# Kernel tuning notes

Hardware: AMD Instinct MI355X
Metric: run time of the kernel (lower is better)

The kernel has to match this reference:

```python
import jax, jax.numpy as jnp
import numpy as np

N = 100000      # nodes
E = 1600000     # edges
IN = 64         # in_channels
ED = 16         # edge_dim
HID = 64        # hidden_dim
L = 5           # num conv layers
MLPL = 4        # linears per GINE mlp
B = 512         # num graphs
BN_EPS = 1e-5


def _linear_init(key, fan_in, shape):
    bound = 1.0 / np.sqrt(fan_in)
    return jax.random.uniform(key, shape, jnp.float32, -bound, bound)


def setup_inputs() -> dict:
    key = jax.random.key(0)
    ks = jax.random.split(key, 12)
    x = jax.random.normal(ks[0], (N, IN), jnp.float32)
    edge_index = jax.random.randint(ks[1], (2, E), 0, N)
    batch = jnp.sort(jax.random.randint(ks[2], (N,), 0, B))
    edge_attr = jax.random.normal(ks[3], (E, ED), jnp.float32)

    node_W = _linear_init(ks[4], IN, (IN, HID))
    node_b = _linear_init(ks[5], IN, (HID,))
    edge_W = _linear_init(ks[6], ED, (ED, HID))
    edge_b = _linear_init(ks[7], ED, (HID,))
    eps_arr = jnp.zeros((L,), jnp.float32)           # train_eps init = 0
    mlp_W = _linear_init(ks[8], HID, (L, MLPL, HID, HID))
    mlp_b = _linear_init(ks[9], HID, (L, MLPL, HID))
    bn_gamma = jnp.ones((L, HID), jnp.float32)
    bn_beta = jnp.zeros((L, HID), jnp.float32)

    return dict(x=x, edge_attr=edge_attr, node_W=node_W, node_b=node_b,
                edge_W=edge_W, edge_b=edge_b, eps_arr=eps_arr,
                mlp_W=mlp_W, mlp_b=mlp_b, bn_gamma=bn_gamma, bn_beta=bn_beta,
                edge_index=edge_index, batch=batch)


def _mlp(h, Ws, bs):
    # Linear,ReLU,Linear,ReLU,Linear,ReLU,Linear (make_mlp num_layers=4)
    for i in range(MLPL):
        h = h @ Ws[i] + bs[i]
        if i < MLPL - 1:
            h = jax.nn.relu(h)
    return h


def reference(x, edge_attr, node_W, node_b, edge_W, edge_b, eps_arr,
              mlp_W, mlp_b, bn_gamma, bn_beta, edge_index, batch):
    h = x @ node_W + node_b                      # [N, HID]
    e = edge_attr @ edge_W + edge_b              # [E, HID]
    src, dst = edge_index[0], edge_index[1]      # messages src -> dst
    for l in range(L):
        h_res = h
        msg = jax.nn.relu(h[src] + e)            # [E, HID] GINE message
        aggr = jax.ops.segment_sum(msg, dst, num_segments=N)
        h = _mlp((1.0 + eps_arr[l]) * h + aggr, mlp_W[l], mlp_b[l])
        mu = h.mean(axis=0)
        var = h.var(axis=0)                      # biased, matches BN training
        h = (h - mu) * jax.lax.rsqrt(var + BN_EPS) * bn_gamma[l] + bn_beta[l]
        h = jax.nn.relu(h) + h_res
    # global mean pool
    counts = jax.ops.segment_sum(jnp.ones((h.shape[0],), h.dtype), batch, num_segments=B)
    g = jax.ops.segment_sum(h, batch, num_segments=B) / jnp.clip(counts, 1.0)[:, None]
    return g
```

## Files before the change

kernel.cpp:

```cpp
#include <hip/hip_runtime.h>

typedef unsigned short u16;
typedef unsigned int u32;
typedef __attribute__((ext_vector_type(8))) short short8_t;
typedef __attribute__((ext_vector_type(4))) float f32x4;

static_assert(sizeof(short8_t) == 16, "short8 must be 16B");

#define NN 100000
#define NE 1600000

__device__ __forceinline__ float b2f(u16 s) {
    return __builtin_bit_cast(float, ((u32)s) << 16);
}
__device__ __forceinline__ u16 f2b(float f) {
    u32 u = __builtin_bit_cast(u32, f);
    u32 r = u + 0x7fffu + ((u >> 16) & 1u);
    return (u16)(r >> 16);
}
__device__ __forceinline__ u32 pack2(float a, float b) {
    return (u32)f2b(a) | ((u32)f2b(b) << 16);
}
__device__ __forceinline__ float ldf(const void* p, size_t i, int bf) {
    return bf ? b2f(((const u16*)p)[i]) : ((const float*)p)[i];
}

__global__ void detect_kernel(const u32* __restrict__ g, int* __restrict__ flag) {
    if (threadIdx.x == 0 && blockIdx.x == 0) flag[0] = (g[0] == 0x3F803F80u) ? 1 : 0;
}

__global__ __launch_bounds__(256) void hist_kernel(const int* __restrict__ dstA,
                                                   int* __restrict__ cnt, int ne) {
    int e = blockIdx.x * 256 + threadIdx.x;
    if (e >= ne) return;
    atomicAdd(&cnt[dstA[e]], 1);
}

__global__ __launch_bounds__(256) void scanA_kernel(const int* __restrict__ cnt,
                                                    int* __restrict__ tmp,
                                                    int* __restrict__ bsum, int n) {
    __shared__ int sm[2][512];
    int t = threadIdx.x;
    int b0 = blockIdx.x * 512;
    sm[0][t] = (b0 + t < n) ? cnt[b0 + t] : 0;
    sm[0][t + 256] = (b0 + t + 256 < n) ? cnt[b0 + t + 256] : 0;
    int pp = 0;
    for (int off = 1; off < 512; off <<= 1) {
        __syncthreads();
        int j0 = t, j1 = t + 256;
        sm[pp ^ 1][j0] = sm[pp][j0] + (j0 >= off ? sm[pp][j0 - off] : 0);
        sm[pp ^ 1][j1] = sm[pp][j1] + (j1 >= off ? sm[pp][j1 - off] : 0);
        pp ^= 1;
    }
    __syncthreads();
    if (b0 + t < n) tmp[b0 + t] = sm[pp][t];
    if (b0 + t + 256 < n) tmp[b0 + t + 256] = sm[pp][t + 256];
    if (t == 0) bsum[blockIdx.x] = sm[pp][511];
}

__global__ __launch_bounds__(256) void scanB_kernel(int* __restrict__ bsum, int nb) {
    __shared__ int sm[2][256];
    int t = threadIdx.x;
    sm[0][t] = (t < nb) ? bsum[t] : 0;
    int pp = 0;
    for (int off = 1; off < 256; off <<= 1) {
        __syncthreads();
        sm[pp ^ 1][t] = sm[pp][t] + (t >= off ? sm[pp][t - off] : 0);
        pp ^= 1;
    }
    __syncthreads();
    bsum[t] = (t == 0) ? 0 : sm[pp][t - 1];
}

__global__ __launch_bounds__(256) void scanC_kernel(const int* __restrict__ tmp,
                                                    const int* __restrict__ bsum,
                                                    int* __restrict__ row_start, int n, int ne) {
    int i = blockIdx.x * 256 + threadIdx.x;
    if (i > n) return;
    if (i == n) { row_start[n] = ne; return; }
    int off = bsum[i >> 9];
    int loc = i & 511;
    row_start[i] = off + (loc ? tmp[i - 1] : 0);
}

__global__ __launch_bounds__(256) void scatter_kernel(const int* __restrict__ srcA,
                                                      const int* __restrict__ dstA,
                                                      int* __restrict__ cursor,
                                                      int* __restrict__ sperm,
                                                      int* __restrict__ eidx, int ne) {
    int e = blockIdx.x * 256 + threadIdx.x;
    if (e >= ne) return;
    int d = dstA[e];
    int pos = atomicAdd(&cursor[d], 1);
    sperm[pos] = srcA[e];
    eidx[pos] = e;
}

__global__ __launch_bounds__(256) void eperm_kernel(const void* __restrict__ edge_attr,
                                                    const void* __restrict__ eW,
                                                    const void* __restrict__ eB,
                                                    const int* __restrict__ eidx,
                                                    u16* __restrict__ ec, int ne,
                                                    const int* __restrict__ flagp) {
    int bf = flagp[0];
    int lane = threadIdx.x & 63;
    int wid = (blockIdx.x * 256 + threadIdx.x) >> 6;
    int nw = gridDim.x * 4;
    float wt[16];
#pragma unroll
    for (int k = 0; k < 16; k++) wt[k] = ldf(eW, k * 64 + lane, bf);
    float ebv = ldf(eB, lane, bf);
    for (int j = wid; j < ne; j += nw) {
        int eid = eidx[j];
        float eav = 0.f;
        if (lane < 16) eav = ldf(edge_attr, (size_t)eid * 16 + lane, bf);
        float acc = ebv;
#pragma unroll
        for (int k = 0; k < 16; k++) {
            int bits = __builtin_amdgcn_readlane(__builtin_bit_cast(int, eav), k);
            acc += __builtin_bit_cast(float, bits) * wt[k];
        }
        ec[(size_t)j * 64 + lane] = f2b(acc);
    }
}

__global__ __launch_bounds__(256) void eacopy_kernel(const void* __restrict__ edge_attr,
                                                     const int* __restrict__ eidx,
                                                     u16* __restrict__ eap, int ne,
                                                     const int* __restrict__ flagp) {
    int bf = flagp[0];
    long long t = (long long)blockIdx.x * 256 + threadIdx.x;
    if (t >= (long long)ne * 16) return;
    int j = (int)(t >> 4), c = (int)(t & 15);
    int eid = eidx[j];
    eap[(size_t)j * 16 + c] = f2b(ldf(edge_attr, (size_t)eid * 16 + c, bf));
}

template <int NLIN, bool STATS, bool INEXT, bool OUTB16>
__global__ __launch_bounds__(256) void linear64_kernel(const void* in, float* out, u16* outb,
                                                       const void* __restrict__ W, size_t w_off,
                                                       const void* __restrict__ bias,
                                                       size_t b_off, float* stats, int n,
                                                       const int* __restrict__ flagp) {
    __shared__ __align__(16) u16 Ab[2][64 * 72];
    const int bf = flagp[0];
    const int tid = threadIdx.x;
    const int base = blockIdx.x * 64;
    {
        int row = tid >> 2;
        int c0 = (tid & 3) << 4;
        int gr = base + row;
        uint4 w0 = make_uint4(0, 0, 0, 0), w1 = make_uint4(0, 0, 0, 0);
        if (gr < n) {
            if (INEXT && bf) {
                const uint4* gp = (const uint4*)((const u16*)in + (size_t)gr * 64 + c0);
                w0 = gp[0];
                w1 = gp[1];
            } else {
                const float4* gp = (const float4*)((const float*)in + (size_t)gr * 64 + c0);
                float4 q0 = gp[0], q1 = gp[1], q2 = gp[2], q3 = gp[3];
                w0.x = pack2(q0.x, q0.y); w0.y = pack2(q0.z, q0.w);
                w0.z = pack2(q1.x, q1.y); w0.w = pack2(q1.z, q1.w);
                w1.x = pack2(q2.x, q2.y); w1.y = pack2(q2.z, q2.w);
                w1.z = pack2(q3.x, q3.y); w1.w = pack2(q3.z, q3.w);
            }
        }
        uint4* lp = (uint4*)&Ab[0][row * 72 + c0];
        lp[0] = w0;
        lp[1] = w1;
    }
    __syncthreads();
    const int lane = tid & 63;
    const int w = tid >> 6;
    const int m = lane & 15;
    const int quad = lane >> 4;
    const int col = w * 16 + m;
    short8_t bfr[NLIN][2];
    float bsv[NLIN];
#pragma unroll
    for (int i = 0; i < NLIN; i++) {
        bsv[i] = ldf(bias, b_off + i * 64 + col, bf);
#pragma unroll
        for (int kk = 0; kk < 2; kk++) {
            short8_t f;
#pragma unroll
            for (int j = 0; j < 8; j++) {
                size_t idx = w_off + (size_t)i * 4096 + (size_t)(kk * 32 + quad * 8 + j) * 64 + col;
                u16 wv = bf ? ((const u16*)W)[idx] : f2b(((const float*)W)[idx]);
                f[j] = (short)wv;
            }
            bfr[i][kk] = f;
        }
    }
    int cur = 0;
#pragma unroll
    for (int i = 0; i < NLIN; i++) {
        f32x4 accT[4];
#pragma unroll
        for (int t = 0; t < 4; t++) {
            f32x4 acc;
            acc[0] = bsv[i]; acc[1] = bsv[i]; acc[2] = bsv[i]; acc[3] = bsv[i];
            int r = t * 16 + m;
            const u16* ap = &Ab[cur][r * 72 + quad * 8];
            short8_t a0 = *(const short8_t*)ap;
            short8_t a1 = *(const short8_t*)(ap + 32);
            acc = __builtin_amdgcn_mfma_f32_16x16x32_bf16(a0, bfr[i][0], acc, 0, 0, 0);
            acc = __builtin_amdgcn_mfma_f32_16x16x32_bf16(a1, bfr[i][1], acc, 0, 0, 0);
            accT[t] = acc;
        }
        if (i < NLIN - 1) {
#pragma unroll
            for (int t = 0; t < 4; t++)
#pragma unroll
                for (int reg = 0; reg < 4; reg++) {
                    int r2 = t * 16 + quad * 4 + reg;
                    Ab[cur ^ 1][r2 * 72 + col] = f2b(fmaxf(accT[t][reg], 0.f));
                }
            __syncthreads();
            cur ^= 1;
        } else {
            float s1 = 0.f, s2 = 0.f;
#pragma unroll
            for (int t = 0; t < 4; t++)
#pragma unroll
                for (int reg = 0; reg < 4; reg++) {
                    int gr = base + t * 16 + quad * 4 + reg;
                    if (gr < n) {
                        float v = accT[t][reg];
                        out[(size_t)gr * 64 + col] = v;
                        if (OUTB16) outb[(size_t)gr * 64 + col] = f2b(v);
                        if (STATS) { s1 += v; s2 += v * v; }
                    }
                }
            if (STATS) {
                s1 += __shfl_xor(s1, 16, 64);
                s2 += __shfl_xor(s2, 16, 64);
                s1 += __shfl_xor(s1, 32, 64);
                s2 += __shfl_xor(s2, 32, 64);
                if (quad == 0) {
                    atomicAdd(&stats[col], s1);
                    atomicAdd(&stats[64 + col], s2);
                }
            }
        }
    }
}

template <bool EC>
__global__ __launch_bounds__(256) void agg_kernel(const float* __restrict__ h,
                                                  const u16* __restrict__ hb,
                                                  const u16* __restrict__ ec,
                                                  const int* __restrict__ sperm,
                                                  const int* __restrict__ row_start,
                                                  const void* __restrict__ eps_arr, int layer,
                                                  float* __restrict__ u, int n,
                                                  const void* __restrict__ eW,
                                                  const void* __restrict__ eB,
                                                  const int* __restrict__ flagp) {
    int bf = flagp[0];
    int lane = threadIdx.x & 63;
    int i = blockIdx.x * 4 + (threadIdx.x >> 6);
    if (i >= n) return;
    float wt[16];
    float ebv = 0.f;
    if (!EC) {
#pragma unroll
        for (int k = 0; k < 16; k++) wt[k] = ldf(eW, k * 64 + lane, bf);
        ebv = ldf(eB, lane, bf);
    }
    int beg = row_start[i], end = row_start[i + 1];
    float acc = 0.f;
    if (EC) {
        int p = beg;
        for (; p + 1 < end; p += 2) {
            int s0 = sperm[p], s1 = sperm[p + 1];
            float h0 = b2f(hb[(size_t)s0 * 64 + lane]);
            float h1 = b2f(hb[(size_t)s1 * 64 + lane]);
            float e0 = b2f(ec[(size_t)p * 64 + lane]);
            float e1 = b2f(ec[(size_t)p * 64 + 64 + lane]);
            acc += fmaxf(h0 + e0, 0.f);
            acc += fmaxf(h1 + e1, 0.f);
        }
        if (p < end) {
            int s0 = sperm[p];
            acc += fmaxf(b2f(hb[(size_t)s0 * 64 + lane]) + b2f(ec[(size_t)p * 64 + lane]), 0.f);
        }
    } else {
        for (int p = beg; p < end; ++p) {
            int s0 = sperm[p];
            float hv = b2f(hb[(size_t)s0 * 64 + lane]);
            float eav = 0.f;
            if (lane < 16) eav = b2f(ec[(size_t)p * 16 + lane]);
            float ev = ebv;
#pragma unroll
            for (int k = 0; k < 16; k++) {
                int bits = __builtin_amdgcn_readlane(__builtin_bit_cast(int, eav), k);
                ev += __builtin_bit_cast(float, bits) * wt[k];
            }
            acc += fmaxf(hv + ev, 0.f);
        }
    }
    float eps = 1.f + ldf(eps_arr, layer, bf);
    u[(size_t)i * 64 + lane] = eps * h[(size_t)i * 64 + lane] + acc;
}

__global__ __launch_bounds__(256) void bnres_kernel(const float* __restrict__ v,
                                                    float* __restrict__ h, u16* __restrict__ hb,
                                                    const float* __restrict__ stats,
                                                    const void* __restrict__ gamma,
                                                    const void* __restrict__ beta, size_t g_off,
                                                    int n, const int* __restrict__ flagp) {
    int bf = flagp[0];
    int idx = blockIdx.x * 256 + threadIdx.x;
    if (idx >= n * 64) return;
    int f = idx & 63;
    float inv = 1.f / (float)n;
    float mu = stats[f] * inv;
    float var = stats[64 + f] * inv - mu * mu;
    float rs = rsqrtf(var + 1e-5f);
    float ga = ldf(gamma, g_off + f, bf), be = ldf(beta, g_off + f, bf);
    float y = (v[idx] - mu) * rs * ga + be;
    float hn = fmaxf(y, 0.f) + h[idx];
    h[idx] = hn;
    hb[idx] = f2b(hn);
}

__global__ __launch_bounds__(256) void pool1_kernel(const float* __restrict__ h,
                                                    const int* __restrict__ batch,
                                                    float* __restrict__ gsum,
                                                    float* __restrict__ gcnt, int n) {
    int lane = threadIdx.x & 63;
    int s = blockIdx.x * 4 + (threadIdx.x >> 6);
    int start = s * 256;
    if (start >= n) return;
    int endn = min(start + 256, n);
    int cur = -1;
    float acc = 0.f, c = 0.f;
    for (int m = start; m < endn; ++m) {
        int b = batch[m];
        if (b != cur) {
            if (cur >= 0) {
                atomicAdd(&gsum[cur * 64 + lane], acc);
                if (lane == 0) atomicAdd(&gcnt[cur], c);
            }
            cur = b;
            acc = 0.f;
            c = 0.f;
        }
        acc += h[(size_t)m * 64 + lane];
        c += 1.f;
    }
    if (cur >= 0) {
        atomicAdd(&gsum[cur * 64 + lane], acc);
        if (lane == 0) atomicAdd(&gcnt[cur], c);
    }
}

__global__ __launch_bounds__(256) void pool2_kernel(const float* __restrict__ gsum,
                                                    const float* __restrict__ gcnt,
                                                    float* __restrict__ out) {
    int idx = blockIdx.x * 256 + threadIdx.x;
    if (idx >= 512 * 64) return;
    int b = idx >> 6;
    out[idx] = gsum[idx] / fmaxf(gcnt[b], 1.f);
}

extern "C" void kernel_launch(void* const* d_in, const int* in_sizes, int n_in, void* d_out,
                              int out_size, void* d_ws, size_t ws_size, hipStream_t stream) {
    const int N = NN, E = NE;
    const void* x = d_in[0];
    const void* edge_attr = d_in[1];
    const void* node_W = d_in[2];
    const void* node_b = d_in[3];
    const void* edge_W = d_in[4];
    const void* edge_b = d_in[5];
    const void* eps_arr = d_in[6];
    const void* mlp_W = d_in[7];
    const void* mlp_b = d_in[8];
    const void* bn_gamma = d_in[9];
    const void* bn_beta = d_in[10];
    const int* edge_index = (const int*)d_in[11];
    const int* batch = (const int*)d_in[12];

    char* ws = (char*)d_ws;
    size_t o = 0;
    auto take = [&](size_t bytes) -> size_t {
        size_t r = o;
        o = (o + bytes + 255) & ~(size_t)255;
        return r;
    };
    size_t cnt_o = take((size_t)N * 4);
    size_t stats_o = take(5 * 128 * 4);
    size_t gsum_o = take(512 * 64 * 4);
    size_t gcnt_o = take(512 * 4);
    size_t zero_len = o;
    size_t flag_o = take(256);
    size_t row_o = take((size_t)(N + 1) * 4);
    size_t tmp_o = take((size_t)N * 4);
    size_t bsum_o = take(256 * 4);
    size_t cur_o = take((size_t)N * 4);
    size_t sperm_o = take((size_t)E * 4);
    size_t eidx_o = take((size_t)E * 4);
    size_t h_o = take((size_t)N * 64 * 4);
    size_t hb_o = take((size_t)N * 64 * 2);
    size_t u_o = take((size_t)N * 64 * 4);
    size_t ec_o = o;
    bool EC = ws_size >= ec_o + (size_t)E * 64 * 2;

    int* cnt = (int*)(ws + cnt_o);
    float* stats = (float*)(ws + stats_o);
    float* gsum = (float*)(ws + gsum_o);
    float* gcnt = (float*)(ws + gcnt_o);
    int* flagp = (int*)(ws + flag_o);
    int* row = (int*)(ws + row_o);
    int* tmp = (int*)(ws + tmp_o);
    int* bsum = (int*)(ws + bsum_o);
    int* curs = (int*)(ws + cur_o);
    int* sperm = (int*)(ws + sperm_o);
    int* eidx = (int*)(ws + eidx_o);
    float* h = (float*)(ws + h_o);
    u16* hb = (u16*)(ws + hb_o);
    float* u = (float*)(ws + u_o);
    u16* ecache = (u16*)(ws + ec_o);

    hipMemsetAsync(ws, 0, zero_len, stream);
    detect_kernel<<<1, 64, 0, stream>>>((const u32*)bn_gamma, flagp);
    const int* srcA = edge_index;
    const int* dstA = edge_index + E;

    hist_kernel<<<E / 256, 256, 0, stream>>>(dstA, cnt, E);
    int nb = (N + 511) / 512;
    scanA_kernel<<<nb, 256, 0, stream>>>(cnt, tmp, bsum, N);
    scanB_kernel<<<1, 256, 0, stream>>>(bsum, nb);
    scanC_kernel<<<(N + 256) / 256, 256, 0, stream>>>(tmp, bsum, row, N, E);
    hipMemcpyAsync(curs, row, (size_t)N * 4, hipMemcpyDeviceToDevice, stream);
    scatter_kernel<<<E / 256, 256, 0, stream>>>(srcA, dstA, curs, sperm, eidx, E);

    if (EC)
        eperm_kernel<<<2048, 256, 0, stream>>>(edge_attr, edge_W, edge_b, eidx, ecache, E, flagp);
    else
        eacopy_kernel<<<(E * 16) / 256, 256, 0, stream>>>(edge_attr, eidx, ecache, E, flagp);

    linear64_kernel<1, false, true, true><<<(N + 63) / 64, 256, 0, stream>>>(
        x, h, hb, node_W, 0, node_b, 0, nullptr, N, flagp);

    for (int l = 0; l < 5; l++) {
        if (EC)
            agg_kernel<true><<<N / 4, 256, 0, stream>>>(h, hb, ecache, sperm, row, eps_arr, l, u,
                                                        N, edge_W, edge_b, flagp);
        else
            agg_kernel<false><<<N / 4, 256, 0, stream>>>(h, hb, ecache, sperm, row, eps_arr, l, u,
                                                         N, edge_W, edge_b, flagp);
        linear64_kernel<4, true, false, false><<<(N + 63) / 64, 256, 0, stream>>>(
            u, u, nullptr, mlp_W, (size_t)l * 4 * 4096, mlp_b, (size_t)l * 256,
            stats + l * 128, N, flagp);
        bnres_kernel<<<(N * 64) / 256, 256, 0, stream>>>(u, h, hb, stats + l * 128, bn_gamma,
                                                         bn_beta, (size_t)l * 64, N, flagp);
    }

    pool1_kernel<<<(N + 1023) / 1024, 256, 0, stream>>>(h, batch, gsum, gcnt, N);
    pool2_kernel<<<(512 * 64) / 256, 256, 0, stream>>>(gsum, gcnt, (float*)d_out);
}
```

Baseline: 1.790 ms.

## Use MFMA for edge encoder, persist linear blocks, unroll agg, vectorize BN

The edge-feature projection in eperm_kernel now runs as bf16 MFMA over groups of 16 edges instead of per-lane readlane FMAs. linear64_kernel becomes a persistent grid-stride kernel launched with 784 blocks, so each block loads its weights once and reuses them across tiles. The aggregation loop is unrolled by 4 to keep more gathers in flight, and the BN/residual kernel is vectorized to float4 per thread. The edge encoder now rounds the weights and edge_attr to bf16, which costs some precision, and persistent blocks reduce latency hiding across tiles.

```diff
diff --git a/kernel.cpp b/kernel.cpp
--- a/kernel.cpp
+++ b/kernel.cpp
@@ -104,23 +104,59 @@
                                                     const int* __restrict__ flagp) {
     int bf = flagp[0];
     int lane = threadIdx.x & 63;
+    int m = lane & 15;
+    int quad = lane >> 4;
     int wid = (blockIdx.x * 256 + threadIdx.x) >> 6;
     int nw = gridDim.x * 4;
-    float wt[16];
-#pragma unroll
-    for (int k = 0; k < 16; k++) wt[k] = ldf(eW, k * 64 + lane, bf);
-    float ebv = ldf(eB, lane, bf);
-    for (int j = wid; j < ne; j += nw) {
-        int eid = eidx[j];
-        float eav = 0.f;
-        if (lane < 16) eav = ldf(edge_attr, (size_t)eid * 16 + lane, bf);
-        float acc = ebv;
-#pragma unroll
-        for (int k = 0; k < 16; k++) {
-            int bits = __builtin_amdgcn_readlane(__builtin_bit_cast(int, eav), k);
-            acc += __builtin_bit_cast(float, bits) * wt[k];
-        }
-        ec[(size_t)j * 64 + lane] = f2b(acc);
+    short8_t bfr[4];
+    float bsv[4];
+#pragma unroll
+    for (int t = 0; t < 4; t++) {
+        short8_t f;
+#pragma unroll
+        for (int j = 0; j < 8; j++) {
+            int k = quad * 8 + j;
+            u16 wv = 0;
+            if (k < 16) wv = f2b(ldf(eW, (size_t)k * 64 + t * 16 + m, bf));
+            f[j] = (short)wv;
+        }
+        bfr[t] = f;
+        bsv[t] = ldf(eB, t * 16 + m, bf);
+    }
+    int ngroups = (ne + 15) >> 4;
+    for (int g = wid; g < ngroups; g += nw) {
+        int row = g * 16 + m;
+        int eid = (row < ne) ? eidx[row] : 0;
+        short8_t afr = {0, 0, 0, 0, 0, 0, 0, 0};
+        if (quad < 2) {
+            if (bf) {
+                const u16* ap = (const u16*)edge_attr + (size_t)eid * 16 + quad * 8;
+                afr = *(const short8_t*)ap;
+            } else {
+                const float* ap = (const float*)edge_attr + (size_t)eid * 16 + quad * 8;
+                float4 q0 = *(const float4*)ap;
+                float4 q1 = *(const float4*)(ap + 4);
+                afr[0] = (short)f2b(q0.x); afr[1] = (short)f2b(q0.y);
+                afr[2] = (short)f2b(q0.z); afr[3] = (short)f2b(q0.w);
+                afr[4] = (short)f2b(q1.x); afr[5] = (short)f2b(q1.y);
+                afr[6] = (short)f2b(q1.z); afr[7] = (short)f2b(q1.w);
+            }
+        }
+        f32x4 acc[4];
+#pragma unroll
+        for (int t = 0; t < 4; t++) {
+            f32x4 a;
+            a[0] = bsv[t]; a[1] = bsv[t]; a[2] = bsv[t]; a[3] = bsv[t];
+            acc[t] = __builtin_amdgcn_mfma_f32_16x16x32_bf16(afr, bfr[t], a, 0, 0, 0);
+        }
+        int rbase = g * 16 + quad * 4;
+#pragma unroll
+        for (int t = 0; t < 4; t++)
+#pragma unroll
+            for (int r = 0; r < 4; r++) {
+                int rr = rbase + r;
+                if (rr < ne) ec[(size_t)rr * 64 + t * 16 + m] = f2b(acc[t][r]);
+            }
     }
 }
 
@@ -145,31 +181,6 @@
     __shared__ __align__(16) u16 Ab[2][64 * 72];
     const int bf = flagp[0];
     const int tid = threadIdx.x;
-    const int base = blockIdx.x * 64;
-    {
-        int row = tid >> 2;
-        int c0 = (tid & 3) << 4;
-        int gr = base + row;
-        uint4 w0 = make_uint4(0, 0, 0, 0), w1 = make_uint4(0, 0, 0, 0);
-        if (gr < n) {
-            if (INEXT && bf) {
-                const uint4* gp = (const uint4*)((const u16*)in + (size_t)gr * 64 + c0);
-                w0 = gp[0];
-                w1 = gp[1];
-            } else {
-                const float4* gp = (const float4*)((const float*)in + (size_t)gr * 64 + c0);
-                float4 q0 = gp[0], q1 = gp[1], q2 = gp[2], q3 = gp[3];
-                w0.x = pack2(q0.x, q0.y); w0.y = pack2(q0.z, q0.w);
-                w0.z = pack2(q1.x, q1.y); w0.w = pack2(q1.z, q1.w);
-                w1.x = pack2(q2.x, q2.y); w1.y = pack2(q2.z, q2.w);
-                w1.z = pack2(q3.x, q3.y); w1.w = pack2(q3.z, q3.w);
-            }
-        }
-        uint4* lp = (uint4*)&Ab[0][row * 72 + c0];
-        lp[0] = w0;
-        lp[1] = w1;
-    }
-    __syncthreads();
     const int lane = tid & 63;
     const int w = tid >> 6;
     const int m = lane & 15;
@@ -192,54 +203,83 @@
             bfr[i][kk] = f;
         }
     }
-    int cur = 0;
-#pragma unroll
-    for (int i = 0; i < NLIN; i++) {
-        f32x4 accT[4];
-#pragma unroll
-        for (int t = 0; t < 4; t++) {
-            f32x4 acc;
-            acc[0] = bsv[i]; acc[1] = bsv[i]; acc[2] = bsv[i]; acc[3] = bsv[i];
-            int r = t * 16 + m;
-            const u16* ap = &Ab[cur][r * 72 + quad * 8];
-            short8_t a0 = *(const short8_t*)ap;
-            short8_t a1 = *(const short8_t*)(ap + 32);
-            acc = __builtin_amdgcn_mfma_f32_16x16x32_bf16(a0, bfr[i][0], acc, 0, 0, 0);
-            acc = __builtin_amdgcn_mfma_f32_16x16x32_bf16(a1, bfr[i][1], acc, 0, 0, 0);
-            accT[t] = acc;
-        }
-        if (i < NLIN - 1) {
-#pragma unroll
-            for (int t = 0; t < 4; t++)
-#pragma unroll
-                for (int reg = 0; reg < 4; reg++) {
-                    int r2 = t * 16 + quad * 4 + reg;
-                    Ab[cur ^ 1][r2 * 72 + col] = f2b(fmaxf(accT[t][reg], 0.f));
+    const int srow = tid >> 2;
+    const int sc0 = (tid & 3) << 4;
+    const int ntiles = (n + 63) >> 6;
+    for (int tile = blockIdx.x; tile < ntiles; tile += gridDim.x) {
+        const int base = tile * 64;
+        __syncthreads();
+        {
+            int gr = base + srow;
+            uint4 w0 = make_uint4(0, 0, 0, 0), w1 = make_uint4(0, 0, 0, 0);
+            if (gr < n) {
+                if (INEXT && bf) {
+                    const uint4* gp = (const uint4*)((const u16*)in + (size_t)gr * 64 + sc0);
+                    w0 = gp[0];
+                    w1 = gp[1];
+                } else {
+                    const float4* gp = (const float4*)((const float*)in + (size_t)gr * 64 + sc0);
+                    float4 q0 = gp[0], q1 = gp[1], q2 = gp[2], q3 = gp[3];
+                    w0.x = pack2(q0.x, q0.y); w0.y = pack2(q0.z, q0.w);
+                    w0.z = pack2(q1.x, q1.y); w0.w = pack2(q1.z, q1.w);
+                    w1.x = pack2(q2.x, q2.y); w1.y = pack2(q2.z, q2.w);
+                    w1.z = pack2(q3.x, q3.y); w1.w = pack2(q3.z, q3.w);
                 }
-            __syncthreads();
-            cur ^= 1;
-        } else {
-            float s1 = 0.f, s2 = 0.f;
-#pragma unroll
-            for (int t = 0; t < 4; t++)
-#pragma unroll
-                for (int reg = 0; reg < 4; reg++) {
-                    int gr = base + t * 16 + quad * 4 + reg;
-                    if (gr < n) {
-                        float v = accT[t][reg];
-                        out[(size_t)gr * 64 + col] = v;
-                        if (OUTB16) outb[(size_t)gr * 64 + col] = f2b(v);
-                        if (STATS) { s1 += v; s2 += v * v; }
+            }
+            uint4* lp = (uint4*)&Ab[0][srow * 72 + sc0];
+            lp[0] = w0;
+            lp[1] = w1;
+        }
+        __syncthreads();
+        int cur = 0;
+#pragma unroll
+        for (int i = 0; i < NLIN; i++) {
+            f32x4 accT[4];
+#pragma unroll
+            for (int t = 0; t < 4; t++) {
+                f32x4 acc;
+                acc[0] = bsv[i]; acc[1] = bsv[i]; acc[2] = bsv[i]; acc[3] = bsv[i];
+                int r = t * 16 + m;
+                const u16* ap = &Ab[cur][r * 72 + quad * 8];
+                short8_t a0 = *(const short8_t*)ap;
+                short8_t a1 = *(const short8_t*)(ap + 32);
+                acc = __builtin_amdgcn_mfma_f32_16x16x32_bf16(a0, bfr[i][0], acc, 0, 0, 0);
+                acc = __builtin_amdgcn_mfma_f32_16x16x32_bf16(a1, bfr[i][1], acc, 0, 0, 0);
+                accT[t] = acc;
+            }
+            if (i < NLIN - 1) {
+#pragma unroll
+                for (int t = 0; t < 4; t++)
+#pragma unroll
+                    for (int reg = 0; reg < 4; reg++) {
+                        int r2 = t * 16 + quad * 4 + reg;
+                        Ab[cur ^ 1][r2 * 72 + col] = f2b(fmaxf(accT[t][reg], 0.f));
                     }
-                }
-            if (STATS) {
-                s1 += __shfl_xor(s1, 16, 64);
-                s2 += __shfl_xor(s2, 16, 64);
-                s1 += __shfl_xor(s1, 32, 64);
-                s2 += __shfl_xor(s2, 32, 64);
-                if (quad == 0) {
-                    atomicAdd(&stats[col], s1);
-                    atomicAdd(&stats[64 + col], s2);
+                __syncthreads();
+                cur ^= 1;
+            } else {
+                float s1 = 0.f, s2 = 0.f;
+#pragma unroll
+                for (int t = 0; t < 4; t++)
+#pragma unroll
+                    for (int reg = 0; reg < 4; reg++) {
+                        int gr = base + t * 16 + quad * 4 + reg;
+                        if (gr < n) {
+                            float v = accT[t][reg];
+                            out[(size_t)gr * 64 + col] = v;
+                            if (OUTB16) outb[(size_t)gr * 64 + col] = f2b(v);
+                            if (STATS) { s1 += v; s2 += v * v; }
+                        }
+                    }
+                if (STATS) {
+                    s1 += __shfl_xor(s1, 16, 64);
+                    s2 += __shfl_xor(s2, 16, 64);
+                    s1 += __shfl_xor(s1, 32, 64);
+                    s2 += __shfl_xor(s2, 32, 64);
+                    if (quad == 0) {
+                        atomicAdd(&stats[col], s1);
+                        atomicAdd(&stats[64 + col], s2);
+                    }
                 }
             }
         }
@@ -272,16 +312,22 @@
     float acc = 0.f;
     if (EC) {
         int p = beg;
-        for (; p + 1 < end; p += 2) {
-            int s0 = sperm[p], s1 = sperm[p + 1];
+        for (; p + 3 < end; p += 4) {
+            int s0 = sperm[p], s1 = sperm[p + 1], s2 = sperm[p + 2], s3 = sperm[p + 3];
             float h0 = b2f(hb[(size_t)s0 * 64 + lane]);
             float h1 = b2f(hb[(size_t)s1 * 64 + lane]);
+            float h2 = b2f(hb[(size_t)s2 * 64 + lane]);
+            float h3 = b2f(hb[(size_t)s3 * 64 + lane]);
             float e0 = b2f(ec[(size_t)p * 64 + lane]);
-            float e1 = b2f(ec[(size_t)p * 64 + 64 + lane]);
+            float e1 = b2f(ec[(size_t)(p + 1) * 64 + lane]);
+            float e2 = b2f(ec[(size_t)(p + 2) * 64 + lane]);
+            float e3 = b2f(ec[(size_t)(p + 3) * 64 + lane]);
             acc += fmaxf(h0 + e0, 0.f);
             acc += fmaxf(h1 + e1, 0.f);
-        }
-        if (p < end) {
+            acc += fmaxf(h2 + e2, 0.f);
+            acc += fmaxf(h3 + e3, 0.f);
+        }
+        for (; p < end; ++p) {
             int s0 = sperm[p];
             acc += fmaxf(b2f(hb[(size_t)s0 * 64 + lane]) + b2f(ec[(size_t)p * 64 + lane]), 0.f);
         }
@@ -311,18 +357,35 @@
                                                     const void* __restrict__ beta, size_t g_off,
                                                     int n, const int* __restrict__ flagp) {
     int bf = flagp[0];
-    int idx = blockIdx.x * 256 + threadIdx.x;
-    if (idx >= n * 64) return;
-    int f = idx & 63;
+    size_t base = ((size_t)blockIdx.x * 256 + threadIdx.x) * 4;
+    if (base >= (size_t)n * 64) return;
+    int f0 = (int)(base & 63);
     float inv = 1.f / (float)n;
-    float mu = stats[f] * inv;
-    float var = stats[64 + f] * inv - mu * mu;
-    float rs = rsqrtf(var + 1e-5f);
-    float ga = ldf(gamma, g_off + f, bf), be = ldf(beta, g_off + f, bf);
-    float y = (v[idx] - mu) * rs * ga + be;
-    float hn = fmaxf(y, 0.f) + h[idx];
-    h[idx] = hn;
-    hb[idx] = f2b(hn);
+    float4 vv = *(const float4*)(v + base);
+    float4 hh = *(const float4*)(h + base);
+    float vs[4] = {vv.x, vv.y, vv.z, vv.w};
+    float hs[4] = {hh.x, hh.y, hh.z, hh.w};
+    float res[4];
+    u16 pb[4];
+#pragma unroll
+    for (int j = 0; j < 4; j++) {
+        int f = f0 + j;
+        float mu = stats[f] * inv;
+        float var = stats[64 + f] * inv - mu * mu;
+        float rs = rsqrtf(var + 1e-5f);
+        float ga = ldf(gamma, g_off + f, bf), be = ldf(beta, g_off + f, bf);
+        float y = (vs[j] - mu) * rs * ga + be;
+        float hn = fmaxf(y, 0.f) + hs[j];
+        res[j] = hn;
+        pb[j] = f2b(hn);
+    }
+    float4 ro;
+    ro.x = res[0]; ro.y = res[1]; ro.z = res[2]; ro.w = res[3];
+    *(float4*)(h + base) = ro;
+    uint2 po;
+    po.x = (u32)pb[0] | ((u32)pb[1] << 16);
+    po.y = (u32)pb[2] | ((u32)pb[3] << 16);
+    *(uint2*)(hb + base) = po;
 }
 
 __global__ __launch_bounds__(256) void pool1_kernel(const float* __restrict__ h,
@@ -441,7 +504,7 @@
     else
         eacopy_kernel<<<(E * 16) / 256, 256, 0, stream>>>(edge_attr, eidx, ecache, E, flagp);
 
-    linear64_kernel<1, false, true, true><<<(N + 63) / 64, 256, 0, stream>>>(
+    linear64_kernel<1, false, true, true><<<784, 256, 0, stream>>>(
         x, h, hb, node_W, 0, node_b, 0, nullptr, N, flagp);
 
     for (int l = 0; l < 5; l++) {
@@ -451,11 +514,11 @@
         else
             agg_kernel<false><<<N / 4, 256, 0, stream>>>(h, hb, ecache, sperm, row, eps_arr, l, u,
                                                          N, edge_W, edge_b, flagp);
-        linear64_kernel<4, true, false, false><<<(N + 63) / 64, 256, 0, stream>>>(
+        linear64_kernel<4, true, false, false><<<784, 256, 0, stream>>>(
             u, u, nullptr, mlp_W, (size_t)l * 4 * 4096, mlp_b, (size_t)l * 256,
             stats + l * 128, N, flagp);
-        bnres_kernel<<<(N * 64) / 256, 256, 0, stream>>>(u, h, hb, stats + l * 128, bn_gamma,
-                                                         bn_beta, (size_t)l * 64, N, flagp);
+        bnres_kernel<<<(N * 64 / 4 + 255) / 256, 256, 0, stream>>>(
+            u, h, hb, stats + l * 128, bn_gamma, bn_beta, (size_t)l * 64, N, flagp);
     }
 
     pool1_kernel<<<(N + 1023) / 1024, 256, 0, stream>>>(h, batch, gsum, gcnt, N);
```

New measurement: 1.629 ms. -9.0%, faster.
